# Kernel optimization log

Hardware: AMD Instinct MI355X
Metric: run time of the kernel (lower is better)

The kernel has to match this reference:

```python
import jax, jax.numpy as jnp
import numpy as np
import math

H = 32      # num attention heads
KV = 8      # num key/value heads
D = 64      # head dim
ROPE_BASE = 10000.0


def _rope_cos_sin(seq_len, dtype):
    inv_freq = 1.0 / (ROPE_BASE ** (jnp.arange(0, D, 2, dtype=jnp.float32) / D))
    t = jnp.arange(seq_len, dtype=jnp.float32)
    freqs = jnp.einsum('i,j->ij', t, inv_freq)          # [S, D/2]
    emb = jnp.concatenate([freqs, freqs], axis=-1)       # [S, D]
    return jnp.cos(emb).astype(dtype)[None, None], jnp.sin(emb).astype(dtype)[None, None]


def _rotate_half(x):
    x1, x2 = x[..., : D // 2], x[..., D // 2:]
    return jnp.concatenate([-x2, x1], axis=-1)


def setup_inputs() -> dict:
    key = jax.random.key(0)
    ks = jax.random.split(key, 5)
    B, S, Hid = 1, 2048, 2048
    hidden_states = jax.random.normal(ks[0], (B, S, Hid), dtype=jnp.float32)
    Wq = jax.random.normal(ks[1], (Hid, H * D), dtype=jnp.float32) * (1.0 / math.sqrt(Hid))
    Wk = jax.random.normal(ks[2], (Hid, KV * D), dtype=jnp.float32) * (1.0 / math.sqrt(Hid))
    Wv = jax.random.normal(ks[3], (Hid, KV * D), dtype=jnp.float32) * (1.0 / math.sqrt(Hid))
    Wo = jax.random.normal(ks[4], (H * D, Hid), dtype=jnp.float32) * (1.0 / math.sqrt(H * D))
    # additive causal mask
    causal = jnp.tril(jnp.ones((S, S), dtype=bool))
    attention_mask = jnp.where(causal, 0.0, -1e9).astype(jnp.float32)[None, None]
    return {"hidden_states": hidden_states, "Wq": Wq, "Wk": Wk, "Wv": Wv,
            "Wo": Wo, "attention_mask": attention_mask}


def reference(hidden_states, Wq, Wk, Wv, Wo, attention_mask):
    B, S, _ = hidden_states.shape
    groups = H // KV
    # projections -> [B, heads, S, D]
    q = (hidden_states @ Wq).reshape(B, S, H, D).transpose(0, 2, 1, 3)
    k = (hidden_states @ Wk).reshape(B, S, KV, D).transpose(0, 2, 1, 3)
    v = (hidden_states @ Wv).reshape(B, S, KV, D).transpose(0, 2, 1, 3)
    # RoPE
    cos, sin = _rope_cos_sin(S, q.dtype)
    q = q * cos + _rotate_half(q) * sin
    k = k * cos + _rotate_half(k) * sin
    # GQA head expansion (repeat_interleave along head axis)
    k = jnp.repeat(k, groups, axis=1)
    v = jnp.repeat(v, groups, axis=1)
    # scaled dot-product attention (eager)
    scores = jnp.einsum('bhqd,bhkd->bhqk', q, k) / math.sqrt(D)
    scores = scores + attention_mask
    probs = jax.nn.softmax(scores.astype(jnp.float32), axis=-1).astype(q.dtype)
    attn = jnp.einsum('bhqk,bhkd->bhqd', probs, v)
    attn = attn.transpose(0, 2, 1, 3).reshape(B, S, H * D)
    return attn @ Wo
```

## Files before the change

### kernel.cpp

```cpp
#include <hip/hip_runtime.h>
#include <hip/hip_bf16.h>
#include <math.h>

#define S_LEN 2048
#define HID   2048
#define NH    32
#define NKV   8
#define HD    64
#define KVW   (NKV * HD)

typedef __attribute__((ext_vector_type(8))) short bf16x8;
typedef __attribute__((ext_vector_type(4))) float f32x4;
typedef unsigned short u16;

__device__ __forceinline__ u16 f2bf(float f) {
    return (u16)((__builtin_bit_cast(unsigned, f) + 0x8000u) >> 16);
}
__device__ __forceinline__ float bf2f(u16 v) {
    unsigned u = ((unsigned)v) << 16;
    return __builtin_bit_cast(float, u);
}
__device__ __forceinline__ unsigned pack2bf(float a, float b) {
    unsigned ua = __builtin_bit_cast(unsigned, a) + 0x8000u;
    unsigned ub = __builtin_bit_cast(unsigned, b) + 0x8000u;
    return (ua >> 16) | (ub & 0xFFFF0000u);
}
__device__ __forceinline__ void stage16(const u16* g, u16* l) {
    __builtin_amdgcn_global_load_lds((const __attribute__((address_space(1))) void*)g,
                                     (__attribute__((address_space(3))) void*)l, 16, 0, 0);
}

__global__ __launch_bounds__(256) void cvt_bf16x8_kernel(const float* __restrict__ X,
                                                         u16* __restrict__ Y, int n8) {
    int i = blockIdx.x * 256 + threadIdx.x;
    if (i >= n8) return;
    const float4* p = (const float4*)(X + (size_t)i * 8);
    float4 a = p[0], b = p[1];
    uint4 o;
    o.x = pack2bf(a.x, a.y);
    o.y = pack2bf(a.z, a.w);
    o.z = pack2bf(b.x, b.y);
    o.w = pack2bf(b.z, b.w);
    *(uint4*)(Y + (size_t)i * 8) = o;
}

__global__ __launch_bounds__(256) void transpose_cvt2(const float* __restrict__ X0,
                                                      u16* __restrict__ Y0,
                                                      const float* __restrict__ X1,
                                                      u16* __restrict__ Y1,
                                                      int R, int C) {
    const float* X = blockIdx.z ? X1 : X0;
    u16* Y = blockIdx.z ? Y1 : Y0;
    __shared__ float T[32][33];
    const int tx = threadIdx.x & 31, ty = threadIdx.x >> 5;
    const int c0 = blockIdx.x * 32, r0 = blockIdx.y * 32;
#pragma unroll
    for (int i = 0; i < 4; i++)
        T[ty + 8 * i][tx] = X[(size_t)(r0 + ty + 8 * i) * C + c0 + tx];
    __syncthreads();
#pragma unroll
    for (int i = 0; i < 4; i++)
        Y[(size_t)(c0 + ty + 8 * i) * R + r0 + tx] = f2bf(T[tx][ty + 8 * i]);
}

template <int WMT, int WNT, int OUTM>
__global__ __launch_bounds__(256) void gemm_bf16(const u16* __restrict__ A,
                                                 const u16* __restrict__ Bt,
                                                 float* __restrict__ C,
                                                 u16* __restrict__ Ct,
                                                 int M, int N, int K) {
    constexpr int BM = 32 * WMT;
    constexpr int BN = 32 * WNT;
    __shared__ u16 As[BM * 32];
    __shared__ u16 Bs[BN * 32];

    const int t = threadIdx.x;
    const int w = t >> 6, lane = t & 63;
    const int qd = lane >> 4, r = lane & 15;
    const int wm = w >> 1, wn = w & 1;
    const int bm = blockIdx.y * BM, bn = blockIdx.x * BN;

    f32x4 acc[WMT][WNT];
#pragma unroll
    for (int i = 0; i < WMT; i++)
#pragma unroll
        for (int j = 0; j < WNT; j++) {
            acc[i][j][0] = 0.f; acc[i][j][1] = 0.f; acc[i][j][2] = 0.f; acc[i][j][3] = 0.f;
        }

    for (int k0 = 0; k0 < K; k0 += 32) {
        __syncthreads();
#pragma unroll
        for (int rd = 0; rd < BM / 64; rd++) {
            int c = rd * 256 + t;
            const u16* g = A + (size_t)(bm + (c >> 2)) * K + k0 + (c & 3) * 8;
            u16* l = As + (size_t)(rd * 256 + w * 64) * 8;
            stage16(g, l);
        }
#pragma unroll
        for (int rd = 0; rd < BN / 64; rd++) {
            int c = rd * 256 + t;
            const u16* g = Bt + (size_t)(bn + (c >> 2)) * K + k0 + (c & 3) * 8;
            u16* l = Bs + (size_t)(rd * 256 + w * 64) * 8;
            stage16(g, l);
        }
        __syncthreads();

        bf16x8 af[WMT], bfr[WNT];
#pragma unroll
        for (int i = 0; i < WMT; i++)
            af[i] = *(const bf16x8*)&As[(wm * WMT * 16 + i * 16 + r) * 32 + qd * 8];
#pragma unroll
        for (int j = 0; j < WNT; j++)
            bfr[j] = *(const bf16x8*)&Bs[(wn * WNT * 16 + j * 16 + r) * 32 + qd * 8];
#pragma unroll
        for (int i = 0; i < WMT; i++)
#pragma unroll
            for (int j = 0; j < WNT; j++)
                acc[i][j] = __builtin_amdgcn_mfma_f32_16x16x32_bf16(af[i], bfr[j], acc[i][j], 0, 0, 0);
    }

    if (OUTM == 2) {
#pragma unroll
        for (int i = 0; i < WMT; i++)
#pragma unroll
            for (int j = 0; j < WNT; j++)
#pragma unroll
                for (int reg = 0; reg < 4; reg++)
                    Ct[(size_t)(bn + wn * WNT * 16 + j * 16 + r) * M
                       + bm + wm * WMT * 16 + i * 16 + qd * 4 + reg] = f2bf(acc[i][j][reg]);
    } else if (OUTM == 1) {
#pragma unroll
        for (int i = 0; i < WMT; i++)
#pragma unroll
            for (int j = 0; j < WNT; j++)
#pragma unroll
                for (int reg = 0; reg < 4; reg++)
                    Ct[(size_t)(bm + wm * WMT * 16 + i * 16 + qd * 4 + reg) * N
                       + bn + wn * WNT * 16 + j * 16 + r] = f2bf(acc[i][j][reg]);
    } else {
#pragma unroll
        for (int i = 0; i < WMT; i++)
#pragma unroll
            for (int j = 0; j < WNT; j++)
#pragma unroll
                for (int reg = 0; reg < 4; reg++)
                    C[(size_t)(bm + wm * WMT * 16 + i * 16 + qd * 4 + reg) * N
                      + bn + wn * WNT * 16 + j * 16 + r] = acc[i][j][reg];
    }
}

__global__ __launch_bounds__(256) void rope_k(const float* __restrict__ Kf,
                                              u16* __restrict__ Kh) {
    int idx = blockIdx.x * blockDim.x + threadIdx.x;
    int s = idx >> 8;
    int rr = idx & 255;
    int head = rr >> 5;
    int j = rr & 31;
    if (s >= S_LEN) return;
    const float LN1E4_OVER_32 = 0.2878231366242596f;
    size_t off = (size_t)s * KVW + head * HD + j;
    float inv = __expf(-(float)j * LN1E4_OVER_32);
    float ang = (float)s * inv;
    float c = cosf(ang), sn = sinf(ang);
    float x1 = Kf[off], x2 = Kf[off + 32];
    Kh[off]      = f2bf(x1 * c - x2 * sn);
    Kh[off + 32] = f2bf(x2 * c + x1 * sn);
}

__global__ __launch_bounds__(256) void attn_mfma(const u16* __restrict__ Qh,
                                                 const u16* __restrict__ K,
                                                 const u16* __restrict__ Vt,
                                                 u16* __restrict__ O) {
    __shared__ u16 Kbuf[2][4096];
    __shared__ u16 Vbuf[4096];
    __shared__ u16 P_lds[4][16][72];

    const int w    = threadIdx.x >> 6;
    const int lane = threadIdx.x & 63;
    const int qd   = lane >> 4;
    const int r    = lane & 15;
    const int qb   = (S_LEN / 64 - 1) - (int)blockIdx.x;
    const int h    = blockIdx.y;
    const int kvh  = h >> 2;
    const int q0w  = qb * 64 + w * 16;

    const u16* qrow = Qh + (size_t)(q0w + r) * (NH * HD) + h * HD;
    bf16x8 qlo = *(const bf16x8*)(qrow + qd * 8);
    bf16x8 qhi = *(const bf16x8*)(qrow + 32 + qd * 8);
    float y1[8], y2[8];
    const float spos = (float)(q0w + r);
    const float LN1E4_OVER_32 = 0.2878231366242596f;
#pragma unroll
    for (int i = 0; i < 8; i++) {
        int jj = qd * 8 + i;
        float x1 = bf2f((u16)qlo[i]);
        float x2 = bf2f((u16)qhi[i]);
        float inv = __expf(-(float)jj * LN1E4_OVER_32);
        float ang = spos * inv;
        float c = cosf(ang), sn = sinf(ang);
        y1[i] = (x1 * c - x2 * sn) * 0.125f;
        y2[i] = (x2 * c + x1 * sn) * 0.125f;
    }
    bf16x8 qfrag[2];
    {
        union { unsigned u[4]; bf16x8 v; } a, b;
#pragma unroll
        for (int i = 0; i < 4; i++) {
            a.u[i] = pack2bf(y1[2 * i], y1[2 * i + 1]);
            b.u[i] = pack2bf(y2[2 * i], y2[2 * i + 1]);
        }
        qfrag[0] = a.v; qfrag[1] = b.v;
    }

    bf16x8 ones;
    {
        union { u16 s[8]; bf16x8 v; } u;
#pragma unroll
        for (int i = 0; i < 8; i++) u.s[i] = 0x3F80;
        ones = u.v;
    }

    f32x4 oacc[4];
    f32x4 lacc;
#pragma unroll
    for (int i = 0; i < 4; i++) { oacc[i][0]=0.f; oacc[i][1]=0.f; oacc[i][2]=0.f; oacc[i][3]=0.f; }
    lacc[0]=0.f; lacc[1]=0.f; lacc[2]=0.f; lacc[3]=0.f;

#define STAGE_K(kt_, buf_)                                                        \
    {                                                                             \
        _Pragma("unroll")                                                         \
        for (int tt = 0; tt < 2; tt++) {                                          \
            int chunk = w * 2 + tt;                                               \
            int nt = chunk >> 1, cc = chunk & 1;                                  \
            const u16* g = K + (size_t)((kt_) * 64 + nt * 16 + r) * KVW           \
                             + kvh * HD + cc * 32 + qd * 8;                       \
            stage16(g, &Kbuf[buf_][chunk * 512]);                                 \
        }                                                                         \
    }
#define STAGE_V(kt_)                                                              \
    {                                                                             \
        _Pragma("unroll")                                                         \
        for (int tt = 0; tt < 2; tt++) {                                          \
            int chunk = w * 2 + tt;                                               \
            int ntd = chunk >> 1, cc = chunk & 1;                                 \
            const u16* g = Vt + (size_t)(kvh * HD + ntd * 16 + r) * S_LEN         \
                              + (kt_) * 64 + cc * 32 + qd * 8;                    \
            stage16(g, &Vbuf[chunk * 512]);                                       \
        }                                                                         \
    }

    STAGE_K(0, 0);
    __syncthreads();
    int cur = 0;

    for (int kt = 0; kt <= qb; kt++) {
        STAGE_V(kt);
        if (kt < qb) STAGE_K(kt + 1, cur ^ 1);

        f32x4 s[4];
#pragma unroll
        for (int nt = 0; nt < 4; nt++) {
            bf16x8 kf0 = *(const bf16x8*)&Kbuf[cur][(nt * 2 + 0) * 512 + lane * 8];
            bf16x8 kf1 = *(const bf16x8*)&Kbuf[cur][(nt * 2 + 1) * 512 + lane * 8];
            f32x4 z; z[0]=0.f; z[1]=0.f; z[2]=0.f; z[3]=0.f;
            z = __builtin_amdgcn_mfma_f32_16x16x32_bf16(qfrag[0], kf0, z, 0, 0, 0);
            s[nt] = __builtin_amdgcn_mfma_f32_16x16x32_bf16(qfrag[1], kf1, z, 0, 0, 0);
        }

        if (kt == qb) {
#pragma unroll
            for (int nt = 0; nt < 4; nt++) {
                int key_local = nt * 16 + r;
#pragma unroll
                for (int reg = 0; reg < 4; reg++) {
                    int q_local = w * 16 + qd * 4 + reg;
                    if (key_local > q_local) s[nt][reg] = -1e30f;
                }
            }
        }

#pragma unroll
        for (int nt = 0; nt < 4; nt++)
#pragma unroll
            for (int reg = 0; reg < 4; reg++)
                P_lds[w][qd * 4 + reg][nt * 16 + r] = f2bf(__expf(s[nt][reg]));

        __syncthreads();

#pragma unroll
        for (int c = 0; c < 2; c++) {
            bf16x8 pf = *(const bf16x8*)&P_lds[w][r][c * 32 + qd * 8];
            lacc = __builtin_amdgcn_mfma_f32_16x16x32_bf16(pf, ones, lacc, 0, 0, 0);
#pragma unroll
            for (int ntd = 0; ntd < 4; ntd++) {
                bf16x8 vf = *(const bf16x8*)&Vbuf[(ntd * 2 + c) * 512 + lane * 8];
                oacc[ntd] = __builtin_amdgcn_mfma_f32_16x16x32_bf16(pf, vf, oacc[ntd], 0, 0, 0);
            }
        }

        __syncthreads();
        cur ^= 1;
    }
#undef STAGE_K
#undef STAGE_V

    float rl[4];
#pragma unroll
    for (int reg = 0; reg < 4; reg++) rl[reg] = 1.f / lacc[reg];
#pragma unroll
    for (int ntd = 0; ntd < 4; ntd++)
#pragma unroll
        for (int reg = 0; reg < 4; reg++)
            O[(size_t)(q0w + qd * 4 + reg) * (NH * HD) + h * HD + ntd * 16 + r] =
                f2bf(oacc[ntd][reg] * rl[reg]);
}

extern "C" void kernel_launch(void* const* d_in, const int* in_sizes, int n_in,
                              void* d_out, int out_size, void* d_ws, size_t ws_size,
                              hipStream_t stream) {
    const float* hidden = (const float*)d_in[0];
    const float* Wq = (const float*)d_in[1];
    const float* Wk = (const float*)d_in[2];
    const float* Wv = (const float*)d_in[3];
    const float* Wo = (const float*)d_in[4];
    float* out = (float*)d_out;

    char* ws = (char*)d_ws;
    const size_t MB = 1024 * 1024;
    u16*   Hh  = (u16*)(ws + 0 * MB);
    u16*   WqT = (u16*)(ws + 8 * MB);
    u16*   WoT = (u16*)(ws + 16 * MB);
    u16*   WkT = (u16*)(ws + 24 * MB);
    u16*   WvT = (u16*)(ws + 26 * MB);
    u16*   Vt  = (u16*)(ws + 28 * MB);
    u16*   Kh  = (u16*)(ws + 30 * MB);
    u16*   Qh  = (u16*)(ws + 32 * MB);
    float* Kb  = (float*)(ws + 40 * MB);
    u16*   Ob  = WqT;

    dim3 blk(256);

    cvt_bf16x8_kernel<<<(S_LEN * HID / 8 + 255) / 256, blk, 0, stream>>>(hidden, Hh, S_LEN * HID / 8);
    transpose_cvt2<<<dim3(HID / 32, HID / 32, 2), blk, 0, stream>>>(Wq, WqT, Wo, WoT, HID, HID);
    transpose_cvt2<<<dim3(KVW / 32, HID / 32, 2), blk, 0, stream>>>(Wk, WkT, Wv, WvT, HID, KVW);

    gemm_bf16<4, 2, 1><<<dim3(HID / 64, S_LEN / 128), blk, 0, stream>>>(Hh, WqT, nullptr, Qh, S_LEN, HID, HID);
    gemm_bf16<2, 2, 0><<<dim3(KVW / 64, S_LEN / 64), blk, 0, stream>>>(Hh, WkT, Kb, nullptr, S_LEN, KVW, HID);
    gemm_bf16<2, 2, 2><<<dim3(KVW / 64, S_LEN / 64), blk, 0, stream>>>(Hh, WvT, nullptr, Vt, S_LEN, KVW, HID);

    rope_k<<<(S_LEN * NKV * 32) / 256, blk, 0, stream>>>(Kb, Kh);

    attn_mfma<<<dim3(S_LEN / 64, NH), blk, 0, stream>>>(Qh, Kh, Vt, Ob);

    gemm_bf16<4, 2, 0><<<dim3(HID / 64, S_LEN / 128), blk, 0, stream>>>(Ob, WoT, out, nullptr, S_LEN, HID, HID);
}
```

Measured before the change: 315.9 us.

## Fuse QKV projection with RoPE epilogue, merge weight transposes, widen attention blocks

```diff
diff --git a/kernel.cpp b/kernel.cpp
--- a/kernel.cpp
+++ b/kernel.cpp
@@ -25,9 +25,9 @@
     unsigned ub = __builtin_bit_cast(unsigned, b) + 0x8000u;
     return (ua >> 16) | (ub & 0xFFFF0000u);
 }
-__device__ __forceinline__ void stage16(const u16* g, u16* l) {
+__device__ __forceinline__ void stage16(const u16* g, u16* lds_base) {
     __builtin_amdgcn_global_load_lds((const __attribute__((address_space(1))) void*)g,
-                                     (__attribute__((address_space(3))) void*)l, 16, 0, 0);
+                                     (__attribute__((address_space(3))) void*)lds_base, 16, 0, 0);
 }
 
 __global__ __launch_bounds__(256) void cvt_bf16x8_kernel(const float* __restrict__ X,
@@ -44,146 +44,159 @@
     *(uint4*)(Y + (size_t)i * 8) = o;
 }
 
-__global__ __launch_bounds__(256) void transpose_cvt2(const float* __restrict__ X0,
-                                                      u16* __restrict__ Y0,
-                                                      const float* __restrict__ X1,
-                                                      u16* __restrict__ Y1,
-                                                      int R, int C) {
-    const float* X = blockIdx.z ? X1 : X0;
-    u16* Y = blockIdx.z ? Y1 : Y0;
+__global__ __launch_bounds__(256) void transpose_cvt4(const float* __restrict__ Wq,
+                                                      const float* __restrict__ Wk,
+                                                      const float* __restrict__ Wv,
+                                                      const float* __restrict__ Wo,
+                                                      u16* __restrict__ WqkvT,
+                                                      u16* __restrict__ WoT) {
+    const float* X; u16* Y; int C;
+    const int z = blockIdx.z;
+    if (z == 0)      { X = Wq; Y = WqkvT;                        C = HID; }
+    else if (z == 1) { X = Wo; Y = WoT;                          C = HID; }
+    else if (z == 2) { X = Wk; Y = WqkvT + (size_t)2048 * HID;   C = KVW; }
+    else             { X = Wv; Y = WqkvT + (size_t)2560 * HID;   C = KVW; }
+    const int c0 = blockIdx.x * 32, r0 = blockIdx.y * 32;
+    if (c0 >= C) return;
     __shared__ float T[32][33];
     const int tx = threadIdx.x & 31, ty = threadIdx.x >> 5;
-    const int c0 = blockIdx.x * 32, r0 = blockIdx.y * 32;
 #pragma unroll
     for (int i = 0; i < 4; i++)
         T[ty + 8 * i][tx] = X[(size_t)(r0 + ty + 8 * i) * C + c0 + tx];
     __syncthreads();
 #pragma unroll
     for (int i = 0; i < 4; i++)
-        Y[(size_t)(c0 + ty + 8 * i) * R + r0 + tx] = f2bf(T[tx][ty + 8 * i]);
-}
-
-template <int WMT, int WNT, int OUTM>
-__global__ __launch_bounds__(256) void gemm_bf16(const u16* __restrict__ A,
-                                                 const u16* __restrict__ Bt,
-                                                 float* __restrict__ C,
-                                                 u16* __restrict__ Ct,
-                                                 int M, int N, int K) {
-    constexpr int BM = 32 * WMT;
-    constexpr int BN = 32 * WNT;
-    __shared__ u16 As[BM * 32];
-    __shared__ u16 Bs[BN * 32];
+        Y[(size_t)(c0 + ty + 8 * i) * HID + r0 + tx] = f2bf(T[tx][ty + 8 * i]);
+}
+
+template <int EPI>
+__global__ __launch_bounds__(256, 4) void gemm_bf16(const u16* __restrict__ A,
+                                                    const u16* __restrict__ Bt,
+                                                    float* __restrict__ C,
+                                                    u16* __restrict__ Qh,
+                                                    u16* __restrict__ Kh,
+                                                    u16* __restrict__ Vt,
+                                                    int K) {
+    __shared__ u16 As[128 * 64];
+    __shared__ u16 Bs[64 * 64];
 
     const int t = threadIdx.x;
     const int w = t >> 6, lane = t & 63;
     const int qd = lane >> 4, r = lane & 15;
     const int wm = w >> 1, wn = w & 1;
-    const int bm = blockIdx.y * BM, bn = blockIdx.x * BN;
-
-    f32x4 acc[WMT][WNT];
-#pragma unroll
-    for (int i = 0; i < WMT; i++)
-#pragma unroll
-        for (int j = 0; j < WNT; j++) {
+    const int bm = blockIdx.y * 128, bn = blockIdx.x * 64;
+    const bool kblk = (EPI == 1) && (bn >= 2048) && (bn < 2560);
+
+    f32x4 acc[4][2];
+#pragma unroll
+    for (int i = 0; i < 4; i++)
+#pragma unroll
+        for (int j = 0; j < 2; j++) {
             acc[i][j][0] = 0.f; acc[i][j][1] = 0.f; acc[i][j][2] = 0.f; acc[i][j][3] = 0.f;
         }
 
-    for (int k0 = 0; k0 < K; k0 += 32) {
+    for (int k0 = 0; k0 < K; k0 += 64) {
         __syncthreads();
 #pragma unroll
-        for (int rd = 0; rd < BM / 64; rd++) {
-            int c = rd * 256 + t;
-            const u16* g = A + (size_t)(bm + (c >> 2)) * K + k0 + (c & 3) * 8;
-            u16* l = As + (size_t)(rd * 256 + w * 64) * 8;
-            stage16(g, l);
-        }
-#pragma unroll
-        for (int rd = 0; rd < BN / 64; rd++) {
-            int c = rd * 256 + t;
-            const u16* g = Bt + (size_t)(bn + (c >> 2)) * K + k0 + (c & 3) * 8;
-            u16* l = Bs + (size_t)(rd * 256 + w * 64) * 8;
-            stage16(g, l);
+        for (int rd = 0; rd < 4; rd++) {
+            int chunk = rd * 4 + w;
+            int tt = chunk >> 1, ss = chunk & 1;
+            const u16* g = A + (size_t)(bm + tt * 16 + r) * K + k0 + ss * 32 + qd * 8;
+            stage16(g, As + chunk * 512);
+        }
+#pragma unroll
+        for (int rd = 0; rd < 2; rd++) {
+            int chunk = rd * 4 + w;
+            int tt = chunk >> 1, ss = chunk & 1;
+            const u16* g = Bt + (size_t)(bn + tt * 16 + r) * K + k0 + ss * 32 + qd * 8;
+            stage16(g, Bs + chunk * 512);
         }
         __syncthreads();
 
-        bf16x8 af[WMT], bfr[WNT];
-#pragma unroll
-        for (int i = 0; i < WMT; i++)
-            af[i] = *(const bf16x8*)&As[(wm * WMT * 16 + i * 16 + r) * 32 + qd * 8];
-#pragma unroll
-        for (int j = 0; j < WNT; j++)
-            bfr[j] = *(const bf16x8*)&Bs[(wn * WNT * 16 + j * 16 + r) * 32 + qd * 8];
-#pragma unroll
-        for (int i = 0; i < WMT; i++)
-#pragma unroll
-            for (int j = 0; j < WNT; j++)
-                acc[i][j] = __builtin_amdgcn_mfma_f32_16x16x32_bf16(af[i], bfr[j], acc[i][j], 0, 0, 0);
-    }
-
-    if (OUTM == 2) {
-#pragma unroll
-        for (int i = 0; i < WMT; i++)
-#pragma unroll
-            for (int j = 0; j < WNT; j++)
+#pragma unroll
+        for (int ss = 0; ss < 2; ss++) {
+            bf16x8 af[4], bfr[2];
+#pragma unroll
+            for (int i = 0; i < 4; i++)
+                af[i] = *(const bf16x8*)&As[((wm * 4 + i) * 2 + ss) * 512 + lane * 8];
+#pragma unroll
+            for (int j = 0; j < 2; j++) {
+                int tile = kblk ? (wn + 2 * j) : (wn * 2 + j);
+                bfr[j] = *(const bf16x8*)&Bs[(tile * 2 + ss) * 512 + lane * 8];
+            }
+#pragma unroll
+            for (int i = 0; i < 4; i++)
+#pragma unroll
+                for (int j = 0; j < 2; j++)
+                    acc[i][j] = __builtin_amdgcn_mfma_f32_16x16x32_bf16(af[i], bfr[j], acc[i][j], 0, 0, 0);
+        }
+    }
+
+    const int row0 = bm + wm * 64;
+    if (EPI == 0) {
+#pragma unroll
+        for (int i = 0; i < 4; i++)
+#pragma unroll
+            for (int j = 0; j < 2; j++)
 #pragma unroll
                 for (int reg = 0; reg < 4; reg++)
-                    Ct[(size_t)(bn + wn * WNT * 16 + j * 16 + r) * M
-                       + bm + wm * WMT * 16 + i * 16 + qd * 4 + reg] = f2bf(acc[i][j][reg]);
-    } else if (OUTM == 1) {
-#pragma unroll
-        for (int i = 0; i < WMT; i++)
-#pragma unroll
-            for (int j = 0; j < WNT; j++)
+                    C[(size_t)(row0 + i * 16 + qd * 4 + reg) * HID + bn + wn * 32 + j * 16 + r] =
+                        acc[i][j][reg];
+    } else if (bn < 2048) {
+#pragma unroll
+        for (int i = 0; i < 4; i++)
+#pragma unroll
+            for (int j = 0; j < 2; j++)
 #pragma unroll
                 for (int reg = 0; reg < 4; reg++)
-                    Ct[(size_t)(bm + wm * WMT * 16 + i * 16 + qd * 4 + reg) * N
-                       + bn + wn * WNT * 16 + j * 16 + r] = f2bf(acc[i][j][reg]);
+                    Qh[(size_t)(row0 + i * 16 + qd * 4 + reg) * HID + bn + wn * 32 + j * 16 + r] =
+                        f2bf(acc[i][j][reg]);
+    } else if (kblk) {
+        const int c0 = wn * 16 + r;
+        const float inv = __expf(-(float)c0 * 0.2878231366242596f);
+#pragma unroll
+        for (int i = 0; i < 4; i++)
+#pragma unroll
+            for (int reg = 0; reg < 4; reg++) {
+                int srow = row0 + i * 16 + qd * 4 + reg;
+                float ang = (float)srow * inv;
+                float cs = cosf(ang), sn = sinf(ang);
+                float k1 = acc[i][0][reg], k2 = acc[i][1][reg];
+                size_t o = (size_t)srow * KVW + (bn - 2048) + c0;
+                Kh[o]      = f2bf(k1 * cs - k2 * sn);
+                Kh[o + 32] = f2bf(k2 * cs + k1 * sn);
+            }
     } else {
 #pragma unroll
-        for (int i = 0; i < WMT; i++)
-#pragma unroll
-            for (int j = 0; j < WNT; j++)
-#pragma unroll
-                for (int reg = 0; reg < 4; reg++)
-                    C[(size_t)(bm + wm * WMT * 16 + i * 16 + qd * 4 + reg) * N
-                      + bn + wn * WNT * 16 + j * 16 + r] = acc[i][j][reg];
-    }
-}
-
-__global__ __launch_bounds__(256) void rope_k(const float* __restrict__ Kf,
-                                              u16* __restrict__ Kh) {
-    int idx = blockIdx.x * blockDim.x + threadIdx.x;
-    int s = idx >> 8;
-    int rr = idx & 255;
-    int head = rr >> 5;
-    int j = rr & 31;
-    if (s >= S_LEN) return;
-    const float LN1E4_OVER_32 = 0.2878231366242596f;
-    size_t off = (size_t)s * KVW + head * HD + j;
-    float inv = __expf(-(float)j * LN1E4_OVER_32);
-    float ang = (float)s * inv;
-    float c = cosf(ang), sn = sinf(ang);
-    float x1 = Kf[off], x2 = Kf[off + 32];
-    Kh[off]      = f2bf(x1 * c - x2 * sn);
-    Kh[off + 32] = f2bf(x2 * c + x1 * sn);
-}
-
-__global__ __launch_bounds__(256) void attn_mfma(const u16* __restrict__ Qh,
-                                                 const u16* __restrict__ K,
-                                                 const u16* __restrict__ Vt,
-                                                 u16* __restrict__ O) {
+        for (int i = 0; i < 4; i++)
+#pragma unroll
+            for (int j = 0; j < 2; j++) {
+                int nrel = (bn - 2560) + wn * 32 + j * 16 + r;
+                int m0 = row0 + i * 16 + qd * 4;
+                ushort4 v;
+                v.x = f2bf(acc[i][j][0]); v.y = f2bf(acc[i][j][1]);
+                v.z = f2bf(acc[i][j][2]); v.w = f2bf(acc[i][j][3]);
+                *(ushort4*)(Vt + (size_t)nrel * S_LEN + m0) = v;
+            }
+    }
+}
+
+__global__ __launch_bounds__(512, 6) void attn_mfma(const u16* __restrict__ Qh,
+                                                    const u16* __restrict__ K,
+                                                    const u16* __restrict__ Vt,
+                                                    u16* __restrict__ O) {
     __shared__ u16 Kbuf[2][4096];
     __shared__ u16 Vbuf[4096];
-    __shared__ u16 P_lds[4][16][72];
+    __shared__ u16 P_lds[8][16][72];
 
     const int w    = threadIdx.x >> 6;
     const int lane = threadIdx.x & 63;
     const int qd   = lane >> 4;
     const int r    = lane & 15;
-    const int qb   = (S_LEN / 64 - 1) - (int)blockIdx.x;
+    const int qb   = 15 - (int)blockIdx.x;
     const int h    = blockIdx.y;
     const int kvh  = h >> 2;
-    const int q0w  = qb * 64 + w * 16;
+    const int q0w  = qb * 128 + w * 16;
 
     const u16* qrow = Qh + (size_t)(q0w + r) * (NH * HD) + h * HD;
     bf16x8 qlo = *(const bf16x8*)(qrow + qd * 8);
@@ -227,36 +240,28 @@
     for (int i = 0; i < 4; i++) { oacc[i][0]=0.f; oacc[i][1]=0.f; oacc[i][2]=0.f; oacc[i][3]=0.f; }
     lacc[0]=0.f; lacc[1]=0.f; lacc[2]=0.f; lacc[3]=0.f;
 
+    const int ktmax = 2 * qb + 1;
+
 #define STAGE_K(kt_, buf_)                                                        \
     {                                                                             \
-        _Pragma("unroll")                                                         \
-        for (int tt = 0; tt < 2; tt++) {                                          \
-            int chunk = w * 2 + tt;                                               \
-            int nt = chunk >> 1, cc = chunk & 1;                                  \
-            const u16* g = K + (size_t)((kt_) * 64 + nt * 16 + r) * KVW           \
-                             + kvh * HD + cc * 32 + qd * 8;                       \
-            stage16(g, &Kbuf[buf_][chunk * 512]);                                 \
-        }                                                                         \
+        const u16* g = K + (size_t)((kt_) * 64 + (w >> 1) * 16 + r) * KVW         \
+                         + kvh * HD + (w & 1) * 32 + qd * 8;                      \
+        stage16(g, &Kbuf[buf_][w * 512]);                                         \
     }
 #define STAGE_V(kt_)                                                              \
     {                                                                             \
-        _Pragma("unroll")                                                         \
-        for (int tt = 0; tt < 2; tt++) {                                          \
-            int chunk = w * 2 + tt;                                               \
-            int ntd = chunk >> 1, cc = chunk & 1;                                 \
-            const u16* g = Vt + (size_t)(kvh * HD + ntd * 16 + r) * S_LEN         \
-                              + (kt_) * 64 + cc * 32 + qd * 8;                    \
-            stage16(g, &Vbuf[chunk * 512]);                                       \
-        }                                                                         \
+        const u16* g = Vt + (size_t)(kvh * HD + (w >> 1) * 16 + r) * S_LEN        \
+                          + (kt_) * 64 + (w & 1) * 32 + qd * 8;                   \
+        stage16(g, &Vbuf[w * 512]);                                               \
     }
 
     STAGE_K(0, 0);
     __syncthreads();
     int cur = 0;
 
-    for (int kt = 0; kt <= qb; kt++) {
+    for (int kt = 0; kt <= ktmax; kt++) {
         STAGE_V(kt);
-        if (kt < qb) STAGE_K(kt + 1, cur ^ 1);
+        if (kt < ktmax) STAGE_K(kt + 1, cur ^ 1);
 
         f32x4 s[4];
 #pragma unroll
@@ -268,14 +273,14 @@
             s[nt] = __builtin_amdgcn_mfma_f32_16x16x32_bf16(qfrag[1], kf1, z, 0, 0, 0);
         }
 
-        if (kt == qb) {
+        if (kt * 64 + 63 > q0w) {
 #pragma unroll
             for (int nt = 0; nt < 4; nt++) {
-                int key_local = nt * 16 + r;
+                int key = kt * 64 + nt * 16 + r;
 #pragma unroll
                 for (int reg = 0; reg < 4; reg++) {
-                    int q_local = w * 16 + qd * 4 + reg;
-                    if (key_local > q_local) s[nt][reg] = -1e30f;
+                    int qg = q0w + qd * 4 + reg;
+                    if (key > qg) s[nt][reg] = -1e30f;
                 }
             }
         }
@@ -328,30 +333,20 @@
 
     char* ws = (char*)d_ws;
     const size_t MB = 1024 * 1024;
-    u16*   Hh  = (u16*)(ws + 0 * MB);
-    u16*   WqT = (u16*)(ws + 8 * MB);
-    u16*   WoT = (u16*)(ws + 16 * MB);
-    u16*   WkT = (u16*)(ws + 24 * MB);
-    u16*   WvT = (u16*)(ws + 26 * MB);
-    u16*   Vt  = (u16*)(ws + 28 * MB);
-    u16*   Kh  = (u16*)(ws + 30 * MB);
-    u16*   Qh  = (u16*)(ws + 32 * MB);
-    float* Kb  = (float*)(ws + 40 * MB);
-    u16*   Ob  = WqT;
-
-    dim3 blk(256);
-
-    cvt_bf16x8_kernel<<<(S_LEN * HID / 8 + 255) / 256, blk, 0, stream>>>(hidden, Hh, S_LEN * HID / 8);
-    transpose_cvt2<<<dim3(HID / 32, HID / 32, 2), blk, 0, stream>>>(Wq, WqT, Wo, WoT, HID, HID);
-    transpose_cvt2<<<dim3(KVW / 32, HID / 32, 2), blk, 0, stream>>>(Wk, WkT, Wv, WvT, HID, KVW);
-
-    gemm_bf16<4, 2, 1><<<dim3(HID / 64, S_LEN / 128), blk, 0, stream>>>(Hh, WqT, nullptr, Qh, S_LEN, HID, HID);
-    gemm_bf16<2, 2, 0><<<dim3(KVW / 64, S_LEN / 64), blk, 0, stream>>>(Hh, WkT, Kb, nullptr, S_LEN, KVW, HID);
-    gemm_bf16<2, 2, 2><<<dim3(KVW / 64, S_LEN / 64), blk, 0, stream>>>(Hh, WvT, nullptr, Vt, S_LEN, KVW, HID);
-
-    rope_k<<<(S_LEN * NKV * 32) / 256, blk, 0, stream>>>(Kb, Kh);
-
-    attn_mfma<<<dim3(S_LEN / 64, NH), blk, 0, stream>>>(Qh, Kh, Vt, Ob);
-
-    gemm_bf16<4, 2, 0><<<dim3(HID / 64, S_LEN / 128), blk, 0, stream>>>(Ob, WoT, out, nullptr, S_LEN, HID, HID);
-}
+    u16* Hh     = (u16*)(ws + 0 * MB);
+    u16* WqkvT  = (u16*)(ws + 8 * MB);
+    u16* WoT    = (u16*)(ws + 20 * MB);
+    u16* Qh     = (u16*)(ws + 28 * MB);
+    u16* Kh     = (u16*)(ws + 36 * MB);
+    u16* Vt     = (u16*)(ws + 38 * MB);
+    u16* Ob     = WqkvT;
+
+    cvt_bf16x8_kernel<<<(S_LEN * HID / 8 + 255) / 256, 256, 0, stream>>>(hidden, Hh, S_LEN * HID / 8);
+    transpose_cvt4<<<dim3(HID / 32, HID / 32, 4), 256, 0, stream>>>(Wq, Wk, Wv, Wo, WqkvT, WoT);
+
+    gemm_bf16<1><<<dim3(3072 / 64, S_LEN / 128), 256, 0, stream>>>(Hh, WqkvT, nullptr, Qh, Kh, Vt, HID);
+
+    attn_mfma<<<dim3(S_LEN / 128, NH), 512, 0, stream>>>(Qh, Kh, Vt, Ob);
+
+    gemm_bf16<0><<<dim3(HID / 64, S_LEN / 128), 256, 0, stream>>>(Ob, WoT, out, nullptr, nullptr, nullptr, HID);
+}
```

New measurement: 285.5 us. 9.6% less time.
